# Optimization experiments

Measured on AMD Instinct MI355X. Metric: run time of the kernel, lower is better.

## Reference

```python
import jax, jax.numpy as jnp
import numpy as np

H = 1024
NH = 16
HD = H // NH
EPS = 1e-5


def _layernorm(x, g, b):
    mu = jnp.mean(x, axis=-1, keepdims=True)
    var = jnp.mean((x - mu) ** 2, axis=-1, keepdims=True)
    return (x - mu) * jax.lax.rsqrt(var + EPS) * g + b


def setup_inputs() -> dict:
    key = jax.random.key(0)
    ks = jax.random.split(key, 12)
    s = lambda fan_in: 1.0 / np.sqrt(fan_in)
    x = jax.random.normal(ks[0], (2, 2048, H), dtype=jnp.float32)
    return {
        "x": x,
        "ln1_g": jnp.ones((H,), jnp.float32),
        "ln1_b": jnp.zeros((H,), jnp.float32),
        "W_qkv": jax.random.uniform(ks[1], (H, 3 * H), jnp.float32, -s(H), s(H)),
        "b_qkv": jax.random.uniform(ks[2], (3 * H,), jnp.float32, -s(H), s(H)),
        "W_out": jax.random.uniform(ks[3], (H, H), jnp.float32, -s(H), s(H)),
        "b_out": jax.random.uniform(ks[4], (H,), jnp.float32, -s(H), s(H)),
        "ln2_g": jnp.ones((H,), jnp.float32),
        "ln2_b": jnp.zeros((H,), jnp.float32),
        "W1": jax.random.uniform(ks[5], (H, 4 * H), jnp.float32, -s(H), s(H)),
        "b1": jax.random.uniform(ks[6], (4 * H,), jnp.float32, -s(H), s(H)),
        "W2": jax.random.uniform(ks[7], (4 * H, H), jnp.float32, -s(4 * H), s(4 * H)),
        "b2": jax.random.uniform(ks[8], (H,), jnp.float32, -s(4 * H), s(4 * H)),
    }


def reference(x, ln1_g, ln1_b, W_qkv, b_qkv, W_out, b_out, ln2_g, ln2_b, W1, b1, W2, b2):
    B, S, _ = x.shape
    residual = x
    h = _layernorm(x, ln1_g, ln1_b)
    qkv = h @ W_qkv + b_qkv                     # [B,S,3H]
    qkv = qkv.reshape(B, S, 3, NH, HD)
    q, k, v = qkv[:, :, 0], qkv[:, :, 1], qkv[:, :, 2]  # [B,S,NH,HD]
    scale = 1.0 / np.sqrt(HD)
    attn = jnp.einsum("bqhd,bkhd->bhqk", q, k) * scale  # [B,NH,S,S]
    attn = jax.nn.softmax(attn, axis=-1)
    out = jnp.einsum("bhqk,bkhd->bqhd", attn, v).reshape(B, S, H)
    x = residual + (out @ W_out + b_out)
    residual = x
    h = _layernorm(x, ln2_g, ln2_b)
    h = jax.nn.gelu(h @ W1 + b1, approximate=False) @ W2 + b2
    return residual + h
```

## Files before the change

kernel.cpp:

```cpp
#include <hip/hip_runtime.h>
#include <hip/hip_bf16.h>
#include <math.h>

#define HDIM 1024
#define SEQ  2048
#define BATCH 2
#define NHEAD 16
#define HEADD 64

typedef short bf16x8 __attribute__((ext_vector_type(8)));
typedef float f32x4  __attribute__((ext_vector_type(4)));
typedef unsigned short u16x8 __attribute__((ext_vector_type(8)));

__device__ __forceinline__ unsigned short f2bf(float f) {
    unsigned u = __float_as_uint(f);
    unsigned r = (u + 0x7FFFu + ((u >> 16) & 1u)) >> 16;
    return (unsigned short)r;
}
__device__ __forceinline__ float b2f(unsigned short s) {
    return __uint_as_float(((unsigned)s) << 16);
}
__device__ __forceinline__ unsigned pk2bf(float lo, float hi) {
    __hip_bfloat162 h = __float22bfloat162_rn(float2{lo, hi});
    unsigned r;
    __builtin_memcpy(&r, &h, 4);
    return r;
}
__device__ __forceinline__ float fexp2(float x) {
#if __has_builtin(__builtin_amdgcn_exp2f)
    return __builtin_amdgcn_exp2f(x);
#else
    return exp2f(x);
#endif
}
__device__ __forceinline__ void gld16(void* lds, const void* g) {
    __builtin_amdgcn_global_load_lds(
        (const __attribute__((address_space(1))) unsigned int*)(g),
        (__attribute__((address_space(3))) unsigned int*)(lds),
        16, 0, 0);
}

#define SWZ(row, chunk) (((row) * 64) + (((chunk) ^ ((row) & 7)) << 3))

__global__ __launch_bounds__(256) void ln_kernel(const float* __restrict__ x,
                                                 const float* __restrict__ gw,
                                                 const float* __restrict__ bw,
                                                 unsigned short* __restrict__ y)
{
    int row = blockIdx.x;
    int t = threadIdx.x;
    const float* xr = x + (size_t)row * HDIM;
    float4 v = *(const float4*)(xr + t * 4);
    float s1 = v.x + v.y + v.z + v.w;
    float s2 = v.x * v.x + v.y * v.y + v.z * v.z + v.w * v.w;
#pragma unroll
    for (int m = 1; m < 64; m <<= 1) {
        s1 += __shfl_xor(s1, m);
        s2 += __shfl_xor(s2, m);
    }
    __shared__ float red[8];
    int wid = t >> 6;
    if ((t & 63) == 0) { red[wid * 2] = s1; red[wid * 2 + 1] = s2; }
    __syncthreads();
    if (t == 0) {
        float a = red[0] + red[2] + red[4] + red[6];
        float b = red[1] + red[3] + red[5] + red[7];
        red[0] = a; red[1] = b;
    }
    __syncthreads();
    float mu  = red[0] * (1.0f / HDIM);
    float var = red[1] * (1.0f / HDIM) - mu * mu;
    float rs  = rsqrtf(var + 1e-5f);
    float4 g4 = *(const float4*)(gw + t * 4);
    float4 b4 = *(const float4*)(bw + t * 4);
    ushort4 o;
    o.x = f2bf((v.x - mu) * rs * g4.x + b4.x);
    o.y = f2bf((v.y - mu) * rs * g4.y + b4.y);
    o.z = f2bf((v.z - mu) * rs * g4.z + b4.z);
    o.w = f2bf((v.w - mu) * rs * g4.w + b4.w);
    *(ushort4*)(y + (size_t)row * HDIM + t * 4) = o;
}

__global__ __launch_bounds__(256) void wconv_kernel(const float* __restrict__ W,
                                                    unsigned short* __restrict__ WT,
                                                    int K, int N)
{
    __shared__ float tile[32][33];
    int n0 = blockIdx.x * 32, k0 = blockIdx.y * 32;
    int t = threadIdx.x, c = t & 31, r = t >> 5;
#pragma unroll
    for (int i = 0; i < 4; ++i)
        tile[r + 8 * i][c] = W[(size_t)(k0 + r + 8 * i) * N + n0 + c];
    __syncthreads();
#pragma unroll
    for (int i = 0; i < 4; ++i)
        WT[(size_t)(n0 + r + 8 * i) * K + k0 + c] = f2bf(tile[c][r + 8 * i]);
}

template <int EPI>
__global__ __launch_bounds__(256, 2) void mgemm(const unsigned short* __restrict__ A,
                                                const unsigned short* __restrict__ BT,
                                                const float* __restrict__ bias,
                                                const float* __restrict__ resid,
                                                float* __restrict__ Cf,
                                                unsigned short* __restrict__ Cb,
                                                int M, int N, int K)
{
    __shared__ char smem[65536];
    int t = threadIdx.x;
    int bn = blockIdx.x * 128, bm = blockIdx.y * 128;
    int l = t & 63, w = t >> 6;
    int wm = w >> 1, wn = w & 1;
    int lrow = l & 15, kq = l >> 4;

    f32x4 acc[4][4];
#pragma unroll
    for (int i = 0; i < 4; ++i)
#pragma unroll
        for (int j = 0; j < 4; ++j) acc[i][j] = {0.f, 0.f, 0.f, 0.f};

    const unsigned short* Ap[4];
    const unsigned short* Bp[4];
    int ld[4];
#pragma unroll
    for (int i = 0; i < 4; ++i) {
        int cid = i * 256 + t;
        int row = cid >> 3, c = cid & 7;
        int gc = (c ^ (row & 7)) << 3;
        Ap[i] = A + (size_t)(bm + row) * K + gc;
        Bp[i] = BT + (size_t)(bn + row) * K + gc;
        ld[i] = cid << 4;
    }

    int nt = K >> 6;
#pragma unroll
    for (int i = 0; i < 4; ++i) {
        gld16(smem + ld[i], Ap[i]);
        gld16(smem + 16384 + ld[i], Bp[i]);
    }
    __syncthreads();

    for (int tk = 0; tk < nt; ++tk) {
        int cur = (tk & 1) << 15;
        if (tk + 1 < nt) {
            int k0 = (tk + 1) << 6;
            int nxt = 32768 - cur;
#pragma unroll
            for (int i = 0; i < 4; ++i) {
                gld16(smem + nxt + ld[i], Ap[i] + k0);
                gld16(smem + nxt + 16384 + ld[i], Bp[i] + k0);
            }
        }
        const unsigned short* sA = (const unsigned short*)(smem + cur);
        const unsigned short* sB = (const unsigned short*)(smem + cur + 16384);
#pragma unroll
        for (int kk = 0; kk < 2; ++kk) {
            bf16x8 af[4], bv[4];
#pragma unroll
            for (int mi = 0; mi < 4; ++mi)
                af[mi] = *(const bf16x8*)(sA + SWZ(wm * 64 + mi * 16 + lrow, kk * 4 + kq));
#pragma unroll
            for (int ni = 0; ni < 4; ++ni)
                bv[ni] = *(const bf16x8*)(sB + SWZ(wn * 64 + ni * 16 + lrow, kk * 4 + kq));
#pragma unroll
            for (int mi = 0; mi < 4; ++mi)
#pragma unroll
                for (int ni = 0; ni < 4; ++ni)
                    acc[mi][ni] = __builtin_amdgcn_mfma_f32_16x16x32_bf16(af[mi], bv[ni], acc[mi][ni], 0, 0, 0);
        }
        __syncthreads();
    }

    int crow = (l >> 4) * 4;
    int ccol = l & 15;
#pragma unroll
    for (int mi = 0; mi < 4; ++mi) {
#pragma unroll
        for (int ni = 0; ni < 4; ++ni) {
            int gcol = bn + wn * 64 + ni * 16 + ccol;
            float bv = bias[gcol];
#pragma unroll
            for (int r = 0; r < 4; ++r) {
                int grow = bm + wm * 64 + mi * 16 + crow + r;
                size_t off = (size_t)grow * N + gcol;
                float v = acc[mi][ni][r] + bv;
                if (EPI == 1) {
                    Cf[off] = v + resid[off];
                } else if (EPI == 2) {
                    v = 0.5f * v * (1.0f + erff(v * 0.70710678118654752f));
                    Cb[off] = f2bf(v);
                } else {
                    Cb[off] = f2bf(v);
                }
            }
        }
    }
}

__global__ __launch_bounds__(256) void mattn(const unsigned short* __restrict__ qkv,
                                             unsigned short* __restrict__ out)
{
    __shared__ unsigned short Qs[64 * 64];
    __shared__ unsigned short Ks[2][64 * 64];
    __shared__ unsigned short Vt[2][64 * 64];
    __shared__ unsigned short Ps[4 * 16 * 64];
    int t = threadIdx.x;
    int w = t >> 6, l = t & 63;
    int lr = l & 15, lh = l >> 4;
    int q0 = blockIdx.x * 64;
    int hh = blockIdx.y, b = blockIdx.z;
    const unsigned short* Qg = qkv + (size_t)b * SEQ * 3072 + hh * 64;
    const unsigned short* Kg = Qg + 1024;
    const unsigned short* Vg = Qg + 2048;

#pragma unroll
    for (int i = 0; i < 2; ++i) {
        int chunkid = (w * 2 + i) * 64 + l;
        int row = chunkid >> 3, c = chunkid & 7;
        gld16(((char*)Qs) + chunkid * 16,
              Qg + (size_t)(q0 + row) * 3072 + ((c ^ (row & 7)) << 3));
    }

    int kr0 = t >> 3, kc0 = t & 7;
    int kr1 = (t + 256) >> 3;
    const unsigned short* Kp0 = Kg + (size_t)kr0 * 3072 + kc0 * 8;
    const unsigned short* Kp1 = Kg + (size_t)kr1 * 3072 + kc0 * 8;
    int kd0 = SWZ(kr0, kc0);
    int kd1 = SWZ(kr1, kc0);
    int vk = (t & 31) * 2;
    int vd0 = ((t >> 5) & 7) * 8;
    const unsigned short* Vp0 = Vg + (size_t)vk * 3072 + vd0;
    const unsigned short* Vp1 = Vp0 + 3072;

    u16x8 k0 = *(const u16x8*)Kp0;
    u16x8 k1 = *(const u16x8*)Kp1;
    u16x8 v0 = *(const u16x8*)Vp0;
    u16x8 v1 = *(const u16x8*)Vp1;
    Kp0 += 64 * 3072; Kp1 += 64 * 3072; Vp0 += 64 * 3072; Vp1 += 64 * 3072;

    __syncthreads();
    bf16x8 qa[2];
#pragma unroll
    for (int ks = 0; ks < 2; ++ks)
        qa[ks] = *(const bf16x8*)(Qs + SWZ(w * 16 + lr, ks * 4 + lh));

    *(u16x8*)(Ks[0] + kd0) = k0;
    *(u16x8*)(Ks[0] + kd1) = k1;
#pragma unroll
    for (int j = 0; j < 8; ++j) {
        int d = vd0 + j;
        unsigned pack = (unsigned)(unsigned short)v0[j] | ((unsigned)(unsigned short)v1[j] << 16);
        *(unsigned*)(Vt[0] + SWZ(d, vk >> 3) + (vk & 7)) = pack;
    }
    k0 = *(const u16x8*)Kp0; k1 = *(const u16x8*)Kp1;
    v0 = *(const u16x8*)Vp0; v1 = *(const u16x8*)Vp1;
    Kp0 += 64 * 3072; Kp1 += 64 * 3072; Vp0 += 64 * 3072; Vp1 += 64 * 3072;
    asm volatile("s_waitcnt lgkmcnt(0)" ::: "memory");
    __builtin_amdgcn_s_barrier();

    f32x4 o[4];
#pragma unroll
    for (int i = 0; i < 4; ++i) o[i] = {0.f, 0.f, 0.f, 0.f};
    float mr = -3.0e38f, lsum = 0.f;
    unsigned short* Pw = Ps + w * (16 * 64);
    const float C = 0.18033688011112042f;

    const int nt = SEQ / 64;
    for (int tt = 0; tt < nt; ++tt) {
        const unsigned short* Kc = Ks[tt & 1];
        const unsigned short* Vc = Vt[tt & 1];

        f32x4 s[4];
#pragma unroll
        for (int ni = 0; ni < 4; ++ni) s[ni] = {0.f, 0.f, 0.f, 0.f};
#pragma unroll
        for (int ks = 0; ks < 2; ++ks) {
#pragma unroll
            for (int ni = 0; ni < 4; ++ni) {
                bf16x8 kb = *(const bf16x8*)(Kc + SWZ(ni * 16 + lr, ks * 4 + lh));
                s[ni] = __builtin_amdgcn_mfma_f32_16x16x32_bf16(kb, qa[ks], s[ni], 0, 0, 0);
            }
        }
        float mx = s[0][0];
#pragma unroll
        for (int ni = 0; ni < 4; ++ni)
#pragma unroll
            for (int r = 0; r < 4; ++r) mx = fmaxf(mx, s[ni][r]);
        mx = fmaxf(mx, __shfl_xor(mx, 16));
        mx = fmaxf(mx, __shfl_xor(mx, 32));
        if (__any(mx > mr + 64.0f)) {
            float mn = fmaxf(mr, mx);
            float corr = fexp2((mr - mn) * C);
            mr = mn;
            lsum *= corr;
            float cr[4];
#pragma unroll
            for (int r = 0; r < 4; ++r) cr[r] = __shfl(corr, lh * 4 + r, 16);
#pragma unroll
            for (int nd = 0; nd < 4; ++nd) {
                o[nd][0] *= cr[0]; o[nd][1] *= cr[1];
                o[nd][2] *= cr[2]; o[nd][3] *= cr[3];
            }
        }
        float mc = mr * C;
        float rsum = 0.f;
#pragma unroll
        for (int ni = 0; ni < 4; ++ni)
#pragma unroll
            for (int r = 0; r < 4; ++r) {
                float p = fexp2(fmaf(s[ni][r], C, -mc));
                s[ni][r] = p;
                rsum += p;
            }
        rsum += __shfl_xor(rsum, 16);
        rsum += __shfl_xor(rsum, 32);
        lsum += rsum;
#pragma unroll
        for (int ni = 0; ni < 4; ++ni)
#pragma unroll
            for (int rp = 0; rp < 2; ++rp) {
                int k = ni * 16 + lh * 4 + rp * 2;
                *(unsigned*)(Pw + SWZ(lr, k >> 3) + (k & 7)) =
                    pk2bf(s[ni][rp * 2], s[ni][rp * 2 + 1]);
            }
#pragma unroll
        for (int ks = 0; ks < 2; ++ks) {
            bf16x8 pa = *(const bf16x8*)(Pw + SWZ(lr, ks * 4 + lh));
#pragma unroll
            for (int nd = 0; nd < 4; ++nd) {
                bf16x8 vb = *(const bf16x8*)(Vc + SWZ(nd * 16 + lr, ks * 4 + lh));
                o[nd] = __builtin_amdgcn_mfma_f32_16x16x32_bf16(pa, vb, o[nd], 0, 0, 0);
            }
        }

        if (tt + 1 < nt) {
            int nb = (tt & 1) ^ 1;
            *(u16x8*)(Ks[nb] + kd0) = k0;
            *(u16x8*)(Ks[nb] + kd1) = k1;
#pragma unroll
            for (int j = 0; j < 8; ++j) {
                int d = vd0 + j;
                unsigned pack = (unsigned)(unsigned short)v0[j] | ((unsigned)(unsigned short)v1[j] << 16);
                *(unsigned*)(Vt[nb] + SWZ(d, vk >> 3) + (vk & 7)) = pack;
            }
            if (tt + 2 < nt) {
                k0 = *(const u16x8*)Kp0; k1 = *(const u16x8*)Kp1;
                v0 = *(const u16x8*)Vp0; v1 = *(const u16x8*)Vp1;
                Kp0 += 64 * 3072; Kp1 += 64 * 3072; Vp0 += 64 * 3072; Vp1 += 64 * 3072;
            }
            asm volatile("s_waitcnt lgkmcnt(0)" ::: "memory");
            __builtin_amdgcn_s_barrier();
        }
    }
    float inv = 1.0f / lsum;
    float ir[4];
#pragma unroll
    for (int r = 0; r < 4; ++r) ir[r] = __shfl(inv, lh * 4 + r, 16);
#pragma unroll
    for (int r = 0; r < 4; ++r) {
        int q = q0 + w * 16 + lh * 4 + r;
#pragma unroll
        for (int nd = 0; nd < 4; ++nd) {
            int d = nd * 16 + lr;
            out[(size_t)((size_t)b * SEQ + q) * HDIM + hh * 64 + d] = f2bf(o[nd][r] * ir[r]);
        }
    }
}

extern "C" void kernel_launch(void* const* d_in, const int* in_sizes, int n_in,
                              void* d_out, int out_size, void* d_ws, size_t ws_size,
                              hipStream_t stream)
{
    const float* x     = (const float*)d_in[0];
    const float* ln1_g = (const float*)d_in[1];
    const float* ln1_b = (const float*)d_in[2];
    const float* W_qkv = (const float*)d_in[3];
    const float* b_qkv = (const float*)d_in[4];
    const float* W_out = (const float*)d_in[5];
    const float* b_out = (const float*)d_in[6];
    const float* ln2_g = (const float*)d_in[7];
    const float* ln2_b = (const float*)d_in[8];
    const float* W1    = (const float*)d_in[9];
    const float* b1    = (const float*)d_in[10];
    const float* W2    = (const float*)d_in[11];
    const float* b2    = (const float*)d_in[12];
    float* out = (float*)d_out;
    char* ws8  = (char*)d_ws;

    const int M = BATCH * SEQ;
    const size_t MB = 1048576;

    unsigned short* hbuf = (unsigned short*)(ws8);
    unsigned short* qkvb = (unsigned short*)(ws8 + 8 * MB);
    unsigned short* attb = (unsigned short*)(ws8 + 32 * MB);
    unsigned short* ffn1 = (unsigned short*)(ws8 + 8 * MB);
    unsigned short* WqT  = (unsigned short*)(ws8 + 40 * MB);
    unsigned short* WoT  = (unsigned short*)(ws8 + 46 * MB);
    unsigned short* W1T  = (unsigned short*)(ws8 + 48 * MB);
    unsigned short* W2T  = (unsigned short*)(ws8 + 56 * MB);

    wconv_kernel<<<dim3(3 * HDIM / 32, HDIM / 32), 256, 0, stream>>>(W_qkv, WqT, HDIM, 3 * HDIM);
    wconv_kernel<<<dim3(HDIM / 32, HDIM / 32), 256, 0, stream>>>(W_out, WoT, HDIM, HDIM);
    wconv_kernel<<<dim3(4 * HDIM / 32, HDIM / 32), 256, 0, stream>>>(W1, W1T, HDIM, 4 * HDIM);
    wconv_kernel<<<dim3(HDIM / 32, 4 * HDIM / 32), 256, 0, stream>>>(W2, W2T, 4 * HDIM, HDIM);

    ln_kernel<<<M, 256, 0, stream>>>(x, ln1_g, ln1_b, hbuf);
    mgemm<0><<<dim3(3 * HDIM / 128, M / 128), 256, 0, stream>>>(hbuf, WqT, b_qkv, nullptr, nullptr, qkvb, M, 3 * HDIM, HDIM);
    mattn<<<dim3(SEQ / 64, NHEAD, BATCH), 256, 0, stream>>>(qkvb, attb);
    mgemm<1><<<dim3(HDIM / 128, M / 128), 256, 0, stream>>>(attb, WoT, b_out, x, out, nullptr, M, HDIM, HDIM);
    ln_kernel<<<M, 256, 0, stream>>>(out, ln2_g, ln2_b, hbuf);
    mgemm<2><<<dim3(4 * HDIM / 128, M / 128), 256, 0, stream>>>(hbuf, W1T, b1, nullptr, nullptr, ffn1, M, 4 * HDIM, HDIM);
    mgemm<1><<<dim3(HDIM / 128, M / 128), 256, 0, stream>>>(ffn1, W2T, b2, out, out, nullptr, M, HDIM, 4 * HDIM);
}
```

Baseline: 255.1 us.

## Widen attention blocks to 128 queries and merge weight conversion launches

The attention kernel now uses 512 threads (8 waves) per block, each block covering 128 query rows. Every K/V tile staged in shared memory is therefore reused by twice as many waves, which halves global K/V traffic and the number of blocks. The per-thread K/V load shrinks accordingly, and the four weight-transpose launches are merged into one kernel that picks the matrix from the block index. The trade-off is fewer blocks in the grid (512) and more shared memory and barrier participants per block, which may reduce occupancy and latency hiding.

```diff
diff --git a/kernel.cpp b/kernel.cpp
--- a/kernel.cpp
+++ b/kernel.cpp
@@ -11,6 +11,7 @@
 typedef short bf16x8 __attribute__((ext_vector_type(8)));
 typedef float f32x4  __attribute__((ext_vector_type(4)));
 typedef unsigned short u16x8 __attribute__((ext_vector_type(8)));
+typedef unsigned short u16x4 __attribute__((ext_vector_type(4)));
 
 __device__ __forceinline__ unsigned short f2bf(float f) {
     unsigned u = __float_as_uint(f);
@@ -81,12 +82,25 @@
     *(ushort4*)(y + (size_t)row * HDIM + t * 4) = o;
 }
 
-__global__ __launch_bounds__(256) void wconv_kernel(const float* __restrict__ W,
-                                                    unsigned short* __restrict__ WT,
-                                                    int K, int N)
+__global__ __launch_bounds__(256) void wconv_all(const float* __restrict__ Wq,
+                                                 const float* __restrict__ Wo,
+                                                 const float* __restrict__ W1,
+                                                 const float* __restrict__ W2,
+                                                 unsigned short* __restrict__ WqT,
+                                                 unsigned short* __restrict__ WoT,
+                                                 unsigned short* __restrict__ W1T,
+                                                 unsigned short* __restrict__ W2T)
 {
+    int bid = blockIdx.x;
+    const float* W; unsigned short* WT; int K, nx, idx;
+    if (bid < 3072)      { W = Wq; WT = WqT; K = 1024; nx = 96;  idx = bid; }
+    else if (bid < 4096) { W = Wo; WT = WoT; K = 1024; nx = 32;  idx = bid - 3072; }
+    else if (bid < 8192) { W = W1; WT = W1T; K = 1024; nx = 128; idx = bid - 4096; }
+    else                 { W = W2; WT = W2T; K = 4096; nx = 32;  idx = bid - 8192; }
+    int N = nx * 32;
+    int n0 = (idx % nx) * 32, k0 = (idx / nx) * 32;
+
     __shared__ float tile[32][33];
-    int n0 = blockIdx.x * 32, k0 = blockIdx.y * 32;
     int t = threadIdx.x, c = t & 31, r = t >> 5;
 #pragma unroll
     for (int i = 0; i < 4; ++i)
@@ -197,17 +211,17 @@
     }
 }
 
-__global__ __launch_bounds__(256) void mattn(const unsigned short* __restrict__ qkv,
+__global__ __launch_bounds__(512) void mattn(const unsigned short* __restrict__ qkv,
                                              unsigned short* __restrict__ out)
 {
-    __shared__ unsigned short Qs[64 * 64];
+    __shared__ unsigned short Qs[128 * 64];
     __shared__ unsigned short Ks[2][64 * 64];
     __shared__ unsigned short Vt[2][64 * 64];
-    __shared__ unsigned short Ps[4 * 16 * 64];
+    __shared__ unsigned short Ps[8 * 16 * 64];
     int t = threadIdx.x;
     int w = t >> 6, l = t & 63;
     int lr = l & 15, lh = l >> 4;
-    int q0 = blockIdx.x * 64;
+    int q0 = blockIdx.x * 128;
     int hh = blockIdx.y, b = blockIdx.z;
     const unsigned short* Qg = qkv + (size_t)b * SEQ * 3072 + hh * 64;
     const unsigned short* Kg = Qg + 1024;
@@ -215,28 +229,24 @@
 
 #pragma unroll
     for (int i = 0; i < 2; ++i) {
-        int chunkid = (w * 2 + i) * 64 + l;
+        int chunkid = i * 512 + t;
         int row = chunkid >> 3, c = chunkid & 7;
         gld16(((char*)Qs) + chunkid * 16,
               Qg + (size_t)(q0 + row) * 3072 + ((c ^ (row & 7)) << 3));
     }
 
     int kr0 = t >> 3, kc0 = t & 7;
-    int kr1 = (t + 256) >> 3;
     const unsigned short* Kp0 = Kg + (size_t)kr0 * 3072 + kc0 * 8;
-    const unsigned short* Kp1 = Kg + (size_t)kr1 * 3072 + kc0 * 8;
     int kd0 = SWZ(kr0, kc0);
-    int kd1 = SWZ(kr1, kc0);
     int vk = (t & 31) * 2;
-    int vd0 = ((t >> 5) & 7) * 8;
+    int vd0 = ((t >> 5) & 15) * 4;
     const unsigned short* Vp0 = Vg + (size_t)vk * 3072 + vd0;
     const unsigned short* Vp1 = Vp0 + 3072;
 
     u16x8 k0 = *(const u16x8*)Kp0;
-    u16x8 k1 = *(const u16x8*)Kp1;
-    u16x8 v0 = *(const u16x8*)Vp0;
-    u16x8 v1 = *(const u16x8*)Vp1;
-    Kp0 += 64 * 3072; Kp1 += 64 * 3072; Vp0 += 64 * 3072; Vp1 += 64 * 3072;
+    u16x4 v0 = *(const u16x4*)Vp0;
+    u16x4 v1 = *(const u16x4*)Vp1;
+    Kp0 += 64 * 3072; Vp0 += 64 * 3072; Vp1 += 64 * 3072;
 
     __syncthreads();
     bf16x8 qa[2];
@@ -245,16 +255,15 @@
         qa[ks] = *(const bf16x8*)(Qs + SWZ(w * 16 + lr, ks * 4 + lh));
 
     *(u16x8*)(Ks[0] + kd0) = k0;
-    *(u16x8*)(Ks[0] + kd1) = k1;
-#pragma unroll
-    for (int j = 0; j < 8; ++j) {
+#pragma unroll
+    for (int j = 0; j < 4; ++j) {
         int d = vd0 + j;
         unsigned pack = (unsigned)(unsigned short)v0[j] | ((unsigned)(unsigned short)v1[j] << 16);
         *(unsigned*)(Vt[0] + SWZ(d, vk >> 3) + (vk & 7)) = pack;
     }
-    k0 = *(const u16x8*)Kp0; k1 = *(const u16x8*)Kp1;
-    v0 = *(const u16x8*)Vp0; v1 = *(const u16x8*)Vp1;
-    Kp0 += 64 * 3072; Kp1 += 64 * 3072; Vp0 += 64 * 3072; Vp1 += 64 * 3072;
+    k0 = *(const u16x8*)Kp0;
+    v0 = *(const u16x4*)Vp0; v1 = *(const u16x4*)Vp1;
+    Kp0 += 64 * 3072; Vp0 += 64 * 3072; Vp1 += 64 * 3072;
     asm volatile("s_waitcnt lgkmcnt(0)" ::: "memory");
     __builtin_amdgcn_s_barrier();
 
@@ -336,17 +345,16 @@
         if (tt + 1 < nt) {
             int nb = (tt & 1) ^ 1;
             *(u16x8*)(Ks[nb] + kd0) = k0;
-            *(u16x8*)(Ks[nb] + kd1) = k1;
-#pragma unroll
-            for (int j = 0; j < 8; ++j) {
+#pragma unroll
+            for (int j = 0; j < 4; ++j) {
                 int d = vd0 + j;
                 unsigned pack = (unsigned)(unsigned short)v0[j] | ((unsigned)(unsigned short)v1[j] << 16);
                 *(unsigned*)(Vt[nb] + SWZ(d, vk >> 3) + (vk & 7)) = pack;
             }
             if (tt + 2 < nt) {
-                k0 = *(const u16x8*)Kp0; k1 = *(const u16x8*)Kp1;
-                v0 = *(const u16x8*)Vp0; v1 = *(const u16x8*)Vp1;
-                Kp0 += 64 * 3072; Kp1 += 64 * 3072; Vp0 += 64 * 3072; Vp1 += 64 * 3072;
+                k0 = *(const u16x8*)Kp0;
+                v0 = *(const u16x4*)Vp0; v1 = *(const u16x4*)Vp1;
+                Kp0 += 64 * 3072; Vp0 += 64 * 3072; Vp1 += 64 * 3072;
             }
             asm volatile("s_waitcnt lgkmcnt(0)" ::: "memory");
             __builtin_amdgcn_s_barrier();
@@ -399,14 +407,11 @@
     unsigned short* W1T  = (unsigned short*)(ws8 + 48 * MB);
     unsigned short* W2T  = (unsigned short*)(ws8 + 56 * MB);
 
-    wconv_kernel<<<dim3(3 * HDIM / 32, HDIM / 32), 256, 0, stream>>>(W_qkv, WqT, HDIM, 3 * HDIM);
-    wconv_kernel<<<dim3(HDIM / 32, HDIM / 32), 256, 0, stream>>>(W_out, WoT, HDIM, HDIM);
-    wconv_kernel<<<dim3(4 * HDIM / 32, HDIM / 32), 256, 0, stream>>>(W1, W1T, HDIM, 4 * HDIM);
-    wconv_kernel<<<dim3(HDIM / 32, 4 * HDIM / 32), 256, 0, stream>>>(W2, W2T, 4 * HDIM, HDIM);
+    wconv_all<<<12288, 256, 0, stream>>>(W_qkv, W_out, W1, W2, WqT, WoT, W1T, W2T);
 
     ln_kernel<<<M, 256, 0, stream>>>(x, ln1_g, ln1_b, hbuf);
     mgemm<0><<<dim3(3 * HDIM / 128, M / 128), 256, 0, stream>>>(hbuf, WqT, b_qkv, nullptr, nullptr, qkvb, M, 3 * HDIM, HDIM);
-    mattn<<<dim3(SEQ / 64, NHEAD, BATCH), 256, 0, stream>>>(qkvb, attb);
+    mattn<<<dim3(SEQ / 128, NHEAD, BATCH), 512, 0, stream>>>(qkvb, attb);
     mgemm<1><<<dim3(HDIM / 128, M / 128), 256, 0, stream>>>(attb, WoT, b_out, x, out, nullptr, M, HDIM, HDIM);
     ln_kernel<<<M, 256, 0, stream>>>(out, ln2_g, ln2_b, hbuf);
     mgemm<2><<<dim3(4 * HDIM / 128, M / 128), 256, 0, stream>>>(hbuf, W1T, b1, nullptr, nullptr, ffn1, M, 4 * HDIM, HDIM);
```

Result: faster. 232.3 us (-9.0%).
